# Kernel tuning notes

Hardware: AMD Instinct MI355X
Metric: run time of the kernel (lower is better)

Reference implementation:

```python
import jax, jax.numpy as jnp
import numpy as np

N = 100000
E = 1600000
IN_DIM = 512
HID = 64
OUT = 2


def gcn_conv(x, src, dst, W, b, n):
    # transform first (PyG GCNConv: x = x @ W, then propagate)
    xt = x @ W  # [n, d_out]
    # add self-loops
    loop = jnp.arange(n, dtype=src.dtype)
    src_sl = jnp.concatenate([src, loop])
    dst_sl = jnp.concatenate([dst, loop])
    # symmetric normalization: deg over destination (col) incl. self-loops
    ones = jnp.ones(src_sl.shape[0], dtype=xt.dtype)
    deg = jax.ops.segment_sum(ones, dst_sl, num_segments=n)
    dis = jnp.where(deg > 0, jax.lax.rsqrt(deg), 0.0)  # deg^-1/2, inf -> 0
    norm = dis[src_sl] * dis[dst_sl]  # [E+n]
    msgs = xt[src_sl] * norm[:, None]  # gather + scale
    out = jax.ops.segment_sum(msgs, dst_sl, num_segments=n)  # scatter-add
    return out + b


def setup_inputs() -> dict:
    key = jax.random.key(0)
    k0, k1, k2, k3, k4, k5 = jax.random.split(key, 6)
    x = jax.random.normal(k0, (N, IN_DIM), dtype=jnp.float32)
    edge_index = jax.random.randint(k1, (2, E), 0, N, dtype=jnp.int64)
    s1 = 1.0 / np.sqrt(IN_DIM)
    s2 = 1.0 / np.sqrt(HID)
    W1 = jax.random.uniform(k2, (IN_DIM, HID), jnp.float32, -s1, s1)
    b1 = jax.random.uniform(k3, (HID,), jnp.float32, -s1, s1)
    W2 = jax.random.uniform(k4, (HID, OUT), jnp.float32, -s2, s2)
    b2 = jax.random.uniform(k5, (OUT,), jnp.float32, -s2, s2)
    return {"x": x, "edge_index": edge_index, "W1": W1, "b1": b1, "W2": W2, "b2": b2}


def reference(x, edge_index, W1, b1, W2, b2):
    src, dst = edge_index[0], edge_index[1]
    h = gcn_conv(x, src, dst, W1, b1, N)
    h = jax.nn.relu(h)
    # dropout is identity in eval mode (training=False)
    h = gcn_conv(h, src, dst, W2, b2, N)
    return jax.nn.log_softmax(h, axis=1)
```

## Files before the change

### kernel.cpp

```cpp
#include <hip/hip_runtime.h>
#include <hip/hip_bf16.h>

#define NN 100000
#define EE 1600000
#define IN_DIM 512
#define HID 64
#define NB1 391
#define NCH 196
#define CHUNK 8192
#define NGEMM 1563

typedef __attribute__((ext_vector_type(8))) short bf16x8;
typedef __attribute__((ext_vector_type(4))) float f32x4;

static __device__ __forceinline__ short f2bf(float f) {
    __hip_bfloat16 h = __float2bfloat16(f);
    return *reinterpret_cast<short*>(&h);
}
static __device__ __forceinline__ float bf2f(unsigned short u) {
    union { unsigned int i; float f; } c; c.i = ((unsigned int)u) << 16;
    return c.f;
}

__global__ __launch_bounds__(256) void pack_hist_kernel(const float* __restrict__ W1,
                                                        bf16x8* __restrict__ W1p,
                                                        const int* __restrict__ dst,
                                                        int* __restrict__ cnt2d) {
    if (blockIdx.x < 16) {
        int t = blockIdx.x * 256 + threadIdx.x;
        int kstep = t >> 8;
        int kb = (t >> 6) & 3;
        int col = t & 63;
        int kbase = kstep * 32 + kb * 8;
        bf16x8 v;
#pragma unroll
        for (int j = 0; j < 8; ++j) v[j] = f2bf(W1[(size_t)(kbase + j) * HID + col]);
        W1p[t] = v;
    } else {
        __shared__ int h[NB1];
        const int c = blockIdx.x - 16;
        const int t = threadIdx.x;
        for (int i = t; i < NB1; i += 256) h[i] = 0;
        __syncthreads();
        const int base = c * CHUNK;
        for (int i = t; i < CHUNK; i += 256) {
            int e = base + i;
            if (e < EE) atomicAdd(&h[dst[e] >> 8], 1);
        }
        __syncthreads();
        for (int i = t; i < NB1; i += 256) cnt2d[c * NB1 + i] = h[i];
    }
}

__global__ __launch_bounds__(256) void scan1b_kernel(const int* __restrict__ cnt2d,
                                                     int* __restrict__ base2d,
                                                     int* __restrict__ coarse) {
    __shared__ int tot[NB1];
    __shared__ int off[NB1 + 1];
    const int t = threadIdx.x;
    for (int i = t; i < NB1; i += 256) {
        int s = 0;
        for (int c = 0; c < NCH; ++c) s += cnt2d[c * NB1 + i];
        tot[i] = s;
    }
    __syncthreads();
    if (t == 0) {
        int run = 0;
        for (int b = 0; b < NB1; ++b) { off[b] = run; run += tot[b]; }
        off[NB1] = run;
    }
    __syncthreads();
    for (int i = t; i < NB1; i += 256) {
        int run = off[i];
        for (int c = 0; c < NCH; ++c) {
            base2d[c * NB1 + i] = run;
            run += cnt2d[c * NB1 + i];
        }
    }
    for (int i = t; i <= NB1; i += 256) coarse[i] = off[i];
}

__global__ __launch_bounds__(256) void scatter1c_kernel(const int* __restrict__ src,
                                                        const int* __restrict__ dst,
                                                        const int* __restrict__ base2d,
                                                        unsigned int* __restrict__ pairs) {
    __shared__ int cur[NB1];
    const int t = threadIdx.x;
    for (int i = t; i < NB1; i += 256) cur[i] = base2d[blockIdx.x * NB1 + i];
    __syncthreads();
    const int base = blockIdx.x * CHUNK;
    for (int i = t; i < CHUNK; i += 256) {
        int e = base + i;
        if (e < EE) {
            int s = src[e], d = dst[e];
            int pos = atomicAdd(&cur[d >> 8], 1);
            pairs[pos] = ((unsigned int)s << 8) | (unsigned int)(d & 255);
        }
    }
}

__global__ __launch_bounds__(256) void sort_gemm_kernel(
        const unsigned int* __restrict__ pairs, const int* __restrict__ coarse,
        int* __restrict__ offsets, int* __restrict__ cursor,
        int* __restrict__ sorted_src, float* __restrict__ dis,
        const float* __restrict__ x, const bf16x8* __restrict__ W1p,
        unsigned short* __restrict__ xt1b) {
    if (blockIdx.x < NB1) {
        __shared__ int sdeg[256];
        __shared__ int sinc[256];
        __shared__ int scur[256];
        const int b = blockIdx.x;
        const int t = threadIdx.x;
        const int n0 = b << 8;
        const int nn = min(256, NN - n0);
        const int e0 = coarse[b], e1 = coarse[b + 1];

        sdeg[t] = 0;
        __syncthreads();
        for (int e = e0 + t; e < e1; e += 256)
            atomicAdd(&sdeg[pairs[e] & 255u], 1);
        __syncthreads();
        sinc[t] = sdeg[t];
        __syncthreads();
        for (int off = 1; off < 256; off <<= 1) {
            int v = (t >= off) ? sinc[t - off] : 0;
            __syncthreads();
            sinc[t] += v;
            __syncthreads();
        }
        int excl = sinc[t] - sdeg[t];
        scur[t] = excl;
        if (t < nn) {
            offsets[n0 + t] = e0 + excl;
            cursor[n0 + t]  = e0 + excl + sdeg[t];
            dis[n0 + t]     = rsqrtf((float)sdeg[t] + 1.0f);
        }
        __syncthreads();
        for (int e = e0 + t; e < e1; e += 256) {
            unsigned int p = pairs[e];
            int pos = atomicAdd(&scur[p & 255u], 1);
            sorted_src[e0 + pos] = (int)(p >> 8);
        }
    } else {
        const int gb = blockIdx.x - NB1;
        const int wave = threadIdx.x >> 6;
        const int lane = threadIdx.x & 63;
        const int r = lane & 15;
        const int kg = lane >> 4;
        const int row0 = gb * 64 + wave * 16;
        const int rowc = min(row0 + r, NN - 1);
        const float* xr = x + (size_t)rowc * IN_DIM;

        f32x4 acc[4] = {};
#pragma unroll
        for (int ks = 0; ks < 16; ++ks) {
            const int k0 = ks * 32 + kg * 8;
            float4 xa = *(const float4*)(xr + k0);
            float4 xb = *(const float4*)(xr + k0 + 4);
            bf16x8 a;
            a[0] = f2bf(xa.x); a[1] = f2bf(xa.y); a[2] = f2bf(xa.z); a[3] = f2bf(xa.w);
            a[4] = f2bf(xb.x); a[5] = f2bf(xb.y); a[6] = f2bf(xb.z); a[7] = f2bf(xb.w);
            const int bbase = (ks * 4 + kg) * 64;
#pragma unroll
            for (int cb = 0; cb < 4; ++cb) {
                bf16x8 bfr = W1p[bbase + cb * 16 + r];
                acc[cb] = __builtin_amdgcn_mfma_f32_16x16x32_bf16(a, bfr, acc[cb], 0, 0, 0);
            }
        }
#pragma unroll
        for (int cb = 0; cb < 4; ++cb) {
#pragma unroll
            for (int reg = 0; reg < 4; ++reg) {
                int ro = row0 + kg * 4 + reg;
                if (ro < NN) xt1b[(size_t)ro * HID + cb * 16 + r] =
                    (unsigned short)f2bf(acc[cb][reg]);
            }
        }
    }
}

__global__ __launch_bounds__(256) void agg1_fused_kernel(
        const int* __restrict__ offsets, const int* __restrict__ cursor,
        const int* __restrict__ sorted_src, const float* __restrict__ dis,
        const unsigned short* __restrict__ xt1b, const float* __restrict__ b1,
        const float* __restrict__ W2, float* __restrict__ xt2) {
    int node = blockIdx.x * 4 + (threadIdx.x >> 6);
    if (node >= NN) return;
    const int lane = threadIdx.x & 63;
    const int grp = lane >> 4;
    const int fl = lane & 15;
    const int beg = offsets[node], end = cursor[node];
    const float dd = dis[node];
    float acc0 = 0.f, acc1 = 0.f, acc2 = 0.f, acc3 = 0.f;

    for (int base = beg; base < end; base += 64) {
        int m = min(64, end - base);
        int s = 0;
        float nd = 0.f;
        if (lane < m) {
            s = sorted_src[base + lane];
            nd = dis[s];
        }
#pragma unroll 4
        for (int jj = 0; jj < m; jj += 4) {
            int j = jj + grp;
            int sj = __shfl(s, j);
            float nj = __shfl(nd, j);
            float w = (j < m) ? nj : 0.f;
            ushort4 v = *(const ushort4*)(xt1b + (size_t)sj * HID + fl * 4);
            acc0 += bf2f(v.x) * w;
            acc1 += bf2f(v.y) * w;
            acc2 += bf2f(v.z) * w;
            acc3 += bf2f(v.w) * w;
        }
    }
    acc0 += __shfl_xor(acc0, 16); acc0 += __shfl_xor(acc0, 32);
    acc1 += __shfl_xor(acc1, 16); acc1 += __shfl_xor(acc1, 32);
    acc2 += __shfl_xor(acc2, 16); acc2 += __shfl_xor(acc2, 32);
    acc3 += __shfl_xor(acc3, 16); acc3 += __shfl_xor(acc3, 32);

    ushort4 xs = *(const ushort4*)(xt1b + (size_t)node * HID + fl * 4);
    float4 bb = *(const float4*)(b1 + fl * 4);
    float d2 = dd * dd;
    float h0 = fmaxf(acc0 * dd + bf2f(xs.x) * d2 + bb.x, 0.f);
    float h1 = fmaxf(acc1 * dd + bf2f(xs.y) * d2 + bb.y, 0.f);
    float h2 = fmaxf(acc2 * dd + bf2f(xs.z) * d2 + bb.z, 0.f);
    float h3 = fmaxf(acc3 * dd + bf2f(xs.w) * d2 + bb.w, 0.f);

    float4 w01 = *(const float4*)(W2 + fl * 8);
    float4 w23 = *(const float4*)(W2 + fl * 8 + 4);
    float a0 = h0 * w01.x + h1 * w01.z + h2 * w23.x + h3 * w23.z;
    float a1 = h0 * w01.y + h1 * w01.w + h2 * w23.y + h3 * w23.w;
    a0 += __shfl_xor(a0, 1); a0 += __shfl_xor(a0, 2);
    a0 += __shfl_xor(a0, 4); a0 += __shfl_xor(a0, 8);
    a1 += __shfl_xor(a1, 1); a1 += __shfl_xor(a1, 2);
    a1 += __shfl_xor(a1, 4); a1 += __shfl_xor(a1, 8);
    if (lane == 0) *(float2*)(xt2 + (size_t)node * 2) = make_float2(a0, a1);
}

__global__ void agg2_final_kernel(const int* __restrict__ offsets, const int* __restrict__ cursor,
                                  const int* __restrict__ sorted_src,
                                  const float* __restrict__ dis,
                                  const float* __restrict__ xt2,
                                  const float* __restrict__ b2,
                                  float* __restrict__ out) {
    int node = blockIdx.x * 256 + threadIdx.x;
    if (node >= NN) return;
    int beg = offsets[node], end = cursor[node];
    float dd = dis[node];
    float d2 = dd * dd;
    float a0 = xt2[(size_t)node * 2 + 0] * d2;
    float a1 = xt2[(size_t)node * 2 + 1] * d2;
    for (int p = beg; p < end; ++p) {
        int s = sorted_src[p];
        float nrm = dis[s] * dd;
        float2 v = *(const float2*)(xt2 + (size_t)s * 2);
        a0 += v.x * nrm;
        a1 += v.y * nrm;
    }
    float v0 = a0 + b2[0], v1 = a1 + b2[1];
    float m = fmaxf(v0, v1);
    float lse = m + logf(expf(v0 - m) + expf(v1 - m));
    out[(size_t)node * 2 + 0] = v0 - lse;
    out[(size_t)node * 2 + 1] = v1 - lse;
}

extern "C" void kernel_launch(void* const* d_in, const int* in_sizes, int n_in,
                              void* d_out, int out_size, void* d_ws, size_t ws_size,
                              hipStream_t stream) {
    const float* x  = (const float*)d_in[0];
    const int* ei   = (const int*)d_in[1];
    const float* W1 = (const float*)d_in[2];
    const float* b1 = (const float*)d_in[3];
    const float* W2 = (const float*)d_in[4];
    const float* b2 = (const float*)d_in[5];
    const int* src = ei;
    const int* dst = ei + EE;
    float* out = (float*)d_out;

    unsigned short* xt1b = (unsigned short*)d_ws;
    float* dis        = (float*)(xt1b + (size_t)NN * HID);
    int*   offsets    = (int*)(dis + NN);
    int*   cursor     = offsets + NN;
    int*   sorted_src = cursor + NN;
    float* xt2        = (float*)(sorted_src + EE);
    bf16x8* W1p       = (bf16x8*)(xt2 + (size_t)NN * 2);
    int*   cnt2d      = (int*)(W1p + 4096);
    int*   base2d     = cnt2d + NCH * NB1;
    int*   coarse     = base2d + NCH * NB1;
    unsigned int* pairs = (unsigned int*)(coarse + NB1 + 1);

    pack_hist_kernel<<<16 + NCH, 256, 0, stream>>>(W1, W1p, dst, cnt2d);
    scan1b_kernel<<<1, 256, 0, stream>>>(cnt2d, base2d, coarse);
    scatter1c_kernel<<<NCH, 256, 0, stream>>>(src, dst, base2d, pairs);
    sort_gemm_kernel<<<NB1 + NGEMM, 256, 0, stream>>>(pairs, coarse, offsets, cursor,
                                                      sorted_src, dis, x, W1p, xt1b);
    agg1_fused_kernel<<<(NN + 3) / 4, 256, 0, stream>>>(offsets, cursor, sorted_src,
                                                        dis, xt1b, b1, W2, xt2);
    agg2_final_kernel<<<(NN + 255) / 256, 256, 0, stream>>>(offsets, cursor, sorted_src,
                                                            dis, xt2, b2, out);
}
```

Before: 182.7 us.

## Merge all stages into one cooperative persistent kernel with grid syncs

Replaces six kernel launches with a single cooperative kernel that separates stages with grid.sync. The GEMM tiles are split across the histogram, scatter and sort phases so the dense transform overlaps the edge-sorting work. The global prefix scan is dropped in favour of fixed per-bucket arenas of 5120 slots, with counts clamped to the arena size. This removes launch gaps and the serial single-block scan, at the cost of grid-sync overhead and a correctness risk if any bucket has more than 5120 edges.

```diff
diff --git a/kernel.cpp b/kernel.cpp
--- a/kernel.cpp
+++ b/kernel.cpp
@@ -1,5 +1,8 @@
 #include <hip/hip_runtime.h>
 #include <hip/hip_bf16.h>
+#include <hip/hip_cooperative_groups.h>
+
+namespace cg = cooperative_groups;
 
 #define NN 100000
 #define EE 1600000
@@ -9,6 +12,10 @@
 #define NCH 196
 #define CHUNK 8192
 #define NGEMM 1563
+#define ARENA 5120
+#define P1G 828
+#define P3G 400
+#define P4G (NGEMM - P1G - P3G)
 
 typedef __attribute__((ext_vector_type(8))) short bf16x8;
 typedef __attribute__((ext_vector_type(4))) float f32x4;
@@ -22,73 +29,82 @@
     return c.f;
 }
 
-__global__ __launch_bounds__(256) void pack_hist_kernel(const float* __restrict__ W1,
-                                                        bf16x8* __restrict__ W1p,
-                                                        const int* __restrict__ dst,
-                                                        int* __restrict__ cnt2d) {
-    if (blockIdx.x < 16) {
-        int t = blockIdx.x * 256 + threadIdx.x;
-        int kstep = t >> 8;
-        int kb = (t >> 6) & 3;
-        int col = t & 63;
-        int kbase = kstep * 32 + kb * 8;
-        bf16x8 v;
-#pragma unroll
-        for (int j = 0; j < 8; ++j) v[j] = f2bf(W1[(size_t)(kbase + j) * HID + col]);
-        W1p[t] = v;
-    } else {
-        __shared__ int h[NB1];
-        const int c = blockIdx.x - 16;
-        const int t = threadIdx.x;
-        for (int i = t; i < NB1; i += 256) h[i] = 0;
-        __syncthreads();
-        const int base = c * CHUNK;
-        for (int i = t; i < CHUNK; i += 256) {
-            int e = base + i;
-            if (e < EE) atomicAdd(&h[dst[e] >> 8], 1);
-        }
-        __syncthreads();
-        for (int i = t; i < NB1; i += 256) cnt2d[c * NB1 + i] = h[i];
-    }
-}
-
-__global__ __launch_bounds__(256) void scan1b_kernel(const int* __restrict__ cnt2d,
-                                                     int* __restrict__ base2d,
-                                                     int* __restrict__ coarse) {
-    __shared__ int tot[NB1];
-    __shared__ int off[NB1 + 1];
+
+__device__ __forceinline__ void do_pack(int t, const float* __restrict__ W1,
+                                        bf16x8* __restrict__ W1p) {
+    int kstep = t >> 8;
+    int kb = (t >> 6) & 3;
+    int col = t & 63;
+    int kbase = kstep * 32 + kb * 8;
+    bf16x8 v;
+#pragma unroll
+    for (int j = 0; j < 8; ++j) v[j] = f2bf(W1[(size_t)(kbase + j) * HID + col]);
+    W1p[t] = v;
+}
+
+__device__ __forceinline__ void do_gemm(int gb, const float* __restrict__ x,
+                                        const bf16x8* __restrict__ W1p,
+                                        unsigned short* __restrict__ xt1b) {
+    const int wave = threadIdx.x >> 6;
+    const int lane = threadIdx.x & 63;
+    const int r = lane & 15;
+    const int kg = lane >> 4;
+    const int row0 = gb * 64 + wave * 16;
+    const int rowc = min(row0 + r, NN - 1);
+    const float* xr = x + (size_t)rowc * IN_DIM;
+
+    f32x4 acc[4] = {};
+#pragma unroll
+    for (int ks = 0; ks < 16; ++ks) {
+        const int k0 = ks * 32 + kg * 8;
+        float4 xa = *(const float4*)(xr + k0);
+        float4 xb = *(const float4*)(xr + k0 + 4);
+        bf16x8 a;
+        a[0] = f2bf(xa.x); a[1] = f2bf(xa.y); a[2] = f2bf(xa.z); a[3] = f2bf(xa.w);
+        a[4] = f2bf(xb.x); a[5] = f2bf(xb.y); a[6] = f2bf(xb.z); a[7] = f2bf(xb.w);
+        const int bbase = (ks * 4 + kg) * 64;
+#pragma unroll
+        for (int cb = 0; cb < 4; ++cb) {
+            bf16x8 bfr = W1p[bbase + cb * 16 + r];
+            acc[cb] = __builtin_amdgcn_mfma_f32_16x16x32_bf16(a, bfr, acc[cb], 0, 0, 0);
+        }
+    }
+#pragma unroll
+    for (int cb = 0; cb < 4; ++cb) {
+#pragma unroll
+        for (int reg = 0; reg < 4; ++reg) {
+            int ro = row0 + kg * 4 + reg;
+            if (ro < NN) xt1b[(size_t)ro * HID + cb * 16 + r] =
+                (unsigned short)f2bf(acc[cb][reg]);
+        }
+    }
+}
+
+__device__ __forceinline__ void do_hist(int c, const int* __restrict__ dst,
+                                        int* __restrict__ cnt2d, int* shm) {
+    int* h = shm;
     const int t = threadIdx.x;
-    for (int i = t; i < NB1; i += 256) {
-        int s = 0;
-        for (int c = 0; c < NCH; ++c) s += cnt2d[c * NB1 + i];
-        tot[i] = s;
-    }
-    __syncthreads();
-    if (t == 0) {
-        int run = 0;
-        for (int b = 0; b < NB1; ++b) { off[b] = run; run += tot[b]; }
-        off[NB1] = run;
-    }
-    __syncthreads();
-    for (int i = t; i < NB1; i += 256) {
-        int run = off[i];
-        for (int c = 0; c < NCH; ++c) {
-            base2d[c * NB1 + i] = run;
-            run += cnt2d[c * NB1 + i];
-        }
-    }
-    for (int i = t; i <= NB1; i += 256) coarse[i] = off[i];
-}
-
-__global__ __launch_bounds__(256) void scatter1c_kernel(const int* __restrict__ src,
-                                                        const int* __restrict__ dst,
-                                                        const int* __restrict__ base2d,
-                                                        unsigned int* __restrict__ pairs) {
-    __shared__ int cur[NB1];
+    for (int i = t; i < NB1; i += 256) h[i] = 0;
+    __syncthreads();
+    const int base = c * CHUNK;
+    for (int i = t; i < CHUNK; i += 256) {
+        int e = base + i;
+        if (e < EE) atomicAdd(&h[dst[e] >> 8], 1);
+    }
+    __syncthreads();
+    for (int i = t; i < NB1; i += 256) cnt2d[c * NB1 + i] = h[i];
+    __syncthreads();
+}
+
+__device__ __forceinline__ void do_scatter(int c, const int* __restrict__ src,
+                                           const int* __restrict__ dst,
+                                           const int* __restrict__ base2d,
+                                           unsigned int* __restrict__ pairs, int* shm) {
+    int* cur = shm;
     const int t = threadIdx.x;
-    for (int i = t; i < NB1; i += 256) cur[i] = base2d[blockIdx.x * NB1 + i];
-    __syncthreads();
-    const int base = blockIdx.x * CHUNK;
+    for (int i = t; i < NB1; i += 256) cur[i] = i * ARENA + base2d[c * NB1 + i];
+    __syncthreads();
+    const int base = c * CHUNK;
     for (int i = t; i < CHUNK; i += 256) {
         int e = base + i;
         if (e < EE) {
@@ -97,94 +113,58 @@
             pairs[pos] = ((unsigned int)s << 8) | (unsigned int)(d & 255);
         }
     }
-}
-
-__global__ __launch_bounds__(256) void sort_gemm_kernel(
-        const unsigned int* __restrict__ pairs, const int* __restrict__ coarse,
-        int* __restrict__ offsets, int* __restrict__ cursor,
-        int* __restrict__ sorted_src, float* __restrict__ dis,
-        const float* __restrict__ x, const bf16x8* __restrict__ W1p,
-        unsigned short* __restrict__ xt1b) {
-    if (blockIdx.x < NB1) {
-        __shared__ int sdeg[256];
-        __shared__ int sinc[256];
-        __shared__ int scur[256];
-        const int b = blockIdx.x;
-        const int t = threadIdx.x;
-        const int n0 = b << 8;
-        const int nn = min(256, NN - n0);
-        const int e0 = coarse[b], e1 = coarse[b + 1];
-
-        sdeg[t] = 0;
+    __syncthreads();
+}
+
+__device__ __forceinline__ void do_sort(int b, const unsigned int* __restrict__ pairs,
+                                        const int* __restrict__ edge_cnt,
+                                        int* __restrict__ offsets, int* __restrict__ cursor,
+                                        int* __restrict__ sorted_src,
+                                        float* __restrict__ dis, int* shm) {
+    int* sdeg = shm;
+    int* sinc = shm + 256;
+    int* scur = shm + 512;
+    const int t = threadIdx.x;
+    const int n0 = b << 8;
+    const int nn = min(256, NN - n0);
+    const int e0 = b * ARENA;
+    const int e1 = e0 + min(edge_cnt[b], ARENA);
+
+    sdeg[t] = 0;
+    __syncthreads();
+    for (int e = e0 + t; e < e1; e += 256)
+        atomicAdd(&sdeg[pairs[e] & 255u], 1);
+    __syncthreads();
+    sinc[t] = sdeg[t];
+    __syncthreads();
+    for (int off = 1; off < 256; off <<= 1) {
+        int v = (t >= off) ? sinc[t - off] : 0;
         __syncthreads();
-        for (int e = e0 + t; e < e1; e += 256)
-            atomicAdd(&sdeg[pairs[e] & 255u], 1);
+        sinc[t] += v;
         __syncthreads();
-        sinc[t] = sdeg[t];
-        __syncthreads();
-        for (int off = 1; off < 256; off <<= 1) {
-            int v = (t >= off) ? sinc[t - off] : 0;
-            __syncthreads();
-            sinc[t] += v;
-            __syncthreads();
-        }
-        int excl = sinc[t] - sdeg[t];
-        scur[t] = excl;
-        if (t < nn) {
-            offsets[n0 + t] = e0 + excl;
-            cursor[n0 + t]  = e0 + excl + sdeg[t];
-            dis[n0 + t]     = rsqrtf((float)sdeg[t] + 1.0f);
-        }
-        __syncthreads();
-        for (int e = e0 + t; e < e1; e += 256) {
-            unsigned int p = pairs[e];
-            int pos = atomicAdd(&scur[p & 255u], 1);
-            sorted_src[e0 + pos] = (int)(p >> 8);
-        }
-    } else {
-        const int gb = blockIdx.x - NB1;
-        const int wave = threadIdx.x >> 6;
-        const int lane = threadIdx.x & 63;
-        const int r = lane & 15;
-        const int kg = lane >> 4;
-        const int row0 = gb * 64 + wave * 16;
-        const int rowc = min(row0 + r, NN - 1);
-        const float* xr = x + (size_t)rowc * IN_DIM;
-
-        f32x4 acc[4] = {};
-#pragma unroll
-        for (int ks = 0; ks < 16; ++ks) {
-            const int k0 = ks * 32 + kg * 8;
-            float4 xa = *(const float4*)(xr + k0);
-            float4 xb = *(const float4*)(xr + k0 + 4);
-            bf16x8 a;
-            a[0] = f2bf(xa.x); a[1] = f2bf(xa.y); a[2] = f2bf(xa.z); a[3] = f2bf(xa.w);
-            a[4] = f2bf(xb.x); a[5] = f2bf(xb.y); a[6] = f2bf(xb.z); a[7] = f2bf(xb.w);
-            const int bbase = (ks * 4 + kg) * 64;
-#pragma unroll
-            for (int cb = 0; cb < 4; ++cb) {
-                bf16x8 bfr = W1p[bbase + cb * 16 + r];
-                acc[cb] = __builtin_amdgcn_mfma_f32_16x16x32_bf16(a, bfr, acc[cb], 0, 0, 0);
-            }
-        }
-#pragma unroll
-        for (int cb = 0; cb < 4; ++cb) {
-#pragma unroll
-            for (int reg = 0; reg < 4; ++reg) {
-                int ro = row0 + kg * 4 + reg;
-                if (ro < NN) xt1b[(size_t)ro * HID + cb * 16 + r] =
-                    (unsigned short)f2bf(acc[cb][reg]);
-            }
-        }
-    }
-}
-
-__global__ __launch_bounds__(256) void agg1_fused_kernel(
-        const int* __restrict__ offsets, const int* __restrict__ cursor,
-        const int* __restrict__ sorted_src, const float* __restrict__ dis,
-        const unsigned short* __restrict__ xt1b, const float* __restrict__ b1,
-        const float* __restrict__ W2, float* __restrict__ xt2) {
-    int node = blockIdx.x * 4 + (threadIdx.x >> 6);
+    }
+    int excl = sinc[t] - sdeg[t];
+    scur[t] = excl;
+    if (t < nn) {
+        offsets[n0 + t] = e0 + excl;
+        cursor[n0 + t]  = e0 + excl + sdeg[t];
+        dis[n0 + t]     = rsqrtf((float)sdeg[t] + 1.0f);
+    }
+    __syncthreads();
+    for (int e = e0 + t; e < e1; e += 256) {
+        unsigned int p = pairs[e];
+        int pos = atomicAdd(&scur[p & 255u], 1);
+        sorted_src[e0 + pos] = (int)(p >> 8);
+    }
+    __syncthreads();
+}
+
+__device__ __forceinline__ void do_agg1(int q, const int* __restrict__ offsets,
+        const int* __restrict__ cursor, const int* __restrict__ sorted_src,
+        const float* __restrict__ dis, const unsigned short* __restrict__ xt1b,
+        const float* __restrict__ b1, const float* __restrict__ W2,
+        float* __restrict__ xt2) {
+    int node = q * 4 + (threadIdx.x >> 6);
     if (node >= NN) return;
     const int lane = threadIdx.x & 63;
     const int grp = lane >> 4;
@@ -238,14 +218,10 @@
     if (lane == 0) *(float2*)(xt2 + (size_t)node * 2) = make_float2(a0, a1);
 }
 
-__global__ void agg2_final_kernel(const int* __restrict__ offsets, const int* __restrict__ cursor,
-                                  const int* __restrict__ sorted_src,
-                                  const float* __restrict__ dis,
-                                  const float* __restrict__ xt2,
-                                  const float* __restrict__ b2,
-                                  float* __restrict__ out) {
-    int node = blockIdx.x * 256 + threadIdx.x;
-    if (node >= NN) return;
+__device__ __forceinline__ void do_agg2(int node, const int* __restrict__ offsets,
+        const int* __restrict__ cursor, const int* __restrict__ sorted_src,
+        const float* __restrict__ dis, const float* __restrict__ xt2,
+        const float* __restrict__ b2, float* __restrict__ out) {
     int beg = offsets[node], end = cursor[node];
     float dd = dis[node];
     float d2 = dd * dd;
@@ -263,6 +239,62 @@
     float lse = m + logf(expf(v0 - m) + expf(v1 - m));
     out[(size_t)node * 2 + 0] = v0 - lse;
     out[(size_t)node * 2 + 1] = v1 - lse;
+}
+
+__global__ __launch_bounds__(256, 4) void gcn_coop(
+        const float* __restrict__ x, const int* __restrict__ src,
+        const int* __restrict__ dst, const float* __restrict__ W1,
+        const float* __restrict__ b1, const float* __restrict__ W2,
+        const float* __restrict__ b2, float* __restrict__ out,
+        unsigned short* __restrict__ xt1b, float* __restrict__ dis,
+        int* __restrict__ offsets, int* __restrict__ cursor,
+        float* __restrict__ xt2, bf16x8* __restrict__ W1p,
+        int* __restrict__ cnt2d, int* __restrict__ base2d,
+        int* __restrict__ edge_cnt, int* __restrict__ sorted_src,
+        unsigned int* __restrict__ pairs) {
+    cg::grid_group grid = cg::this_grid();
+    __shared__ int shm[768];
+    const int nb = gridDim.x;
+    const int nthreads = nb * 256;
+    const int gt = blockIdx.x * 256 + threadIdx.x;
+
+    for (int t = gt; t < 4096; t += nthreads) do_pack(t, W1, W1p);
+    grid.sync();
+
+    for (int u = blockIdx.x; u < NCH + P1G; u += nb) {
+        if (u < NCH) do_hist(u, dst, cnt2d, shm);
+        else         do_gemm(u - NCH, x, W1p, xt1b);
+    }
+    grid.sync();
+
+    for (int i = gt; i < NB1; i += nthreads) {
+        int run = 0;
+        for (int c = 0; c < NCH; ++c) {
+            base2d[c * NB1 + i] = run;
+            run += cnt2d[c * NB1 + i];
+        }
+        edge_cnt[i] = run;
+    }
+    grid.sync();
+
+    for (int u = blockIdx.x; u < NCH + P3G; u += nb) {
+        if (u < NCH) do_scatter(u, src, dst, base2d, pairs, shm);
+        else         do_gemm(P1G + (u - NCH), x, W1p, xt1b);
+    }
+    grid.sync();
+
+    for (int u = blockIdx.x; u < NB1 + P4G; u += nb) {
+        if (u < NB1) do_sort(u, pairs, edge_cnt, offsets, cursor, sorted_src, dis, shm);
+        else         do_gemm(P1G + P3G + (u - NB1), x, W1p, xt1b);
+    }
+    grid.sync();
+
+    for (int q = blockIdx.x; q < (NN + 3) / 4; q += nb)
+        do_agg1(q, offsets, cursor, sorted_src, dis, xt1b, b1, W2, xt2);
+    grid.sync();
+
+    for (int n = gt; n < NN; n += nthreads)
+        do_agg2(n, offsets, cursor, sorted_src, dis, xt2, b2, out);
 }
 
 extern "C" void kernel_launch(void* const* d_in, const int* in_sizes, int n_in,
@@ -282,21 +314,26 @@
     float* dis        = (float*)(xt1b + (size_t)NN * HID);
     int*   offsets    = (int*)(dis + NN);
     int*   cursor     = offsets + NN;
-    int*   sorted_src = cursor + NN;
-    float* xt2        = (float*)(sorted_src + EE);
+    float* xt2        = (float*)(cursor + NN);
     bf16x8* W1p       = (bf16x8*)(xt2 + (size_t)NN * 2);
     int*   cnt2d      = (int*)(W1p + 4096);
     int*   base2d     = cnt2d + NCH * NB1;
-    int*   coarse     = base2d + NCH * NB1;
-    unsigned int* pairs = (unsigned int*)(coarse + NB1 + 1);
-
-    pack_hist_kernel<<<16 + NCH, 256, 0, stream>>>(W1, W1p, dst, cnt2d);
-    scan1b_kernel<<<1, 256, 0, stream>>>(cnt2d, base2d, coarse);
-    scatter1c_kernel<<<NCH, 256, 0, stream>>>(src, dst, base2d, pairs);
-    sort_gemm_kernel<<<NB1 + NGEMM, 256, 0, stream>>>(pairs, coarse, offsets, cursor,
-                                                      sorted_src, dis, x, W1p, xt1b);
-    agg1_fused_kernel<<<(NN + 3) / 4, 256, 0, stream>>>(offsets, cursor, sorted_src,
-                                                        dis, xt1b, b1, W2, xt2);
-    agg2_final_kernel<<<(NN + 255) / 256, 256, 0, stream>>>(offsets, cursor, sorted_src,
-                                                            dis, xt2, b2, out);
-}
+    int*   edge_cnt   = base2d + NCH * NB1;
+    int*   sorted_src = edge_cnt + NB1;
+    unsigned int* pairs = (unsigned int*)(sorted_src + (size_t)NB1 * ARENA);
+
+    int nbpc = 0;
+    if (hipOccupancyMaxActiveBlocksPerMultiprocessor(&nbpc, gcn_coop, 256, 0) != hipSuccess
+        || nbpc < 1) nbpc = 2;
+    if (nbpc > 8) nbpc = 8;
+    int grid = 256 * nbpc;
+    if (grid > 2048) grid = 2048;
+
+    void* args[] = {
+        (void*)&x, (void*)&src, (void*)&dst, (void*)&W1, (void*)&b1, (void*)&W2,
+        (void*)&b2, (void*)&out, (void*)&xt1b, (void*)&dis, (void*)&offsets,
+        (void*)&cursor, (void*)&xt2, (void*)&W1p, (void*)&cnt2d, (void*)&base2d,
+        (void*)&edge_cnt, (void*)&sorted_src, (void*)&pairs
+    };
+    hipLaunchCooperativeKernel((void*)gcn_coop, dim3(grid), dim3(256), args, 0, stream);
+}
```

New measurement: 680.7 us (median of 2 runs). 3.73x slower.

## Drop serial scan kernel via fixed-size bucket arenas and split GEMM across scatter/sort

Applied to the files above, without the earlier changes.

Removes the single-block prefix-scan kernel: each scatter block now computes its own per-bucket offset by scanning the histogram column. Buckets are placed in fixed-capacity arenas of ARENA slots instead of packed offsets. Part of the bf16 MFMA feature GEMM is moved into the scatter launch so it runs alongside scatter, and the rest stays with the sort. This removes a serial launch and balances GEMM work across two kernels. The risk is that edges beyond arena capacity are silently dropped, which is only safe for near-uniform destination distributions.

```diff
diff --git a/kernel.cpp b/kernel.cpp
--- a/kernel.cpp
+++ b/kernel.cpp
@@ -9,6 +9,9 @@
 #define NCH 196
 #define CHUNK 8192
 #define NGEMM 1563
+#define ARENA 5120
+#define GA 800
+#define GB (NGEMM - GA)
 
 typedef __attribute__((ext_vector_type(8))) short bf16x8;
 typedef __attribute__((ext_vector_type(4))) float f32x4;
@@ -20,6 +23,44 @@
 static __device__ __forceinline__ float bf2f(unsigned short u) {
     union { unsigned int i; float f; } c; c.i = ((unsigned int)u) << 16;
     return c.f;
+}
+
+__device__ __forceinline__ void do_gemm(int gb, const float* __restrict__ x,
+                                        const bf16x8* __restrict__ W1p,
+                                        unsigned short* __restrict__ xt1b) {
+    const int wave = threadIdx.x >> 6;
+    const int lane = threadIdx.x & 63;
+    const int r = lane & 15;
+    const int kg = lane >> 4;
+    const int row0 = gb * 64 + wave * 16;
+    const int rowc = min(row0 + r, NN - 1);
+    const float* xr = x + (size_t)rowc * IN_DIM;
+
+    f32x4 acc[4] = {};
+#pragma unroll
+    for (int ks = 0; ks < 16; ++ks) {
+        const int k0 = ks * 32 + kg * 8;
+        float4 xa = *(const float4*)(xr + k0);
+        float4 xb = *(const float4*)(xr + k0 + 4);
+        bf16x8 a;
+        a[0] = f2bf(xa.x); a[1] = f2bf(xa.y); a[2] = f2bf(xa.z); a[3] = f2bf(xa.w);
+        a[4] = f2bf(xb.x); a[5] = f2bf(xb.y); a[6] = f2bf(xb.z); a[7] = f2bf(xb.w);
+        const int bbase = (ks * 4 + kg) * 64;
+#pragma unroll
+        for (int cb = 0; cb < 4; ++cb) {
+            bf16x8 bfr = W1p[bbase + cb * 16 + r];
+            acc[cb] = __builtin_amdgcn_mfma_f32_16x16x32_bf16(a, bfr, acc[cb], 0, 0, 0);
+        }
+    }
+#pragma unroll
+    for (int cb = 0; cb < 4; ++cb) {
+#pragma unroll
+        for (int reg = 0; reg < 4; ++reg) {
+            int ro = row0 + kg * 4 + reg;
+            if (ro < NN) xt1b[(size_t)ro * HID + cb * 16 + r] =
+                (unsigned short)f2bf(acc[cb][reg]);
+        }
+    }
 }
 
 __global__ __launch_bounds__(256) void pack_hist_kernel(const float* __restrict__ W1,
@@ -52,55 +93,45 @@
     }
 }
 
-__global__ __launch_bounds__(256) void scan1b_kernel(const int* __restrict__ cnt2d,
-                                                     int* __restrict__ base2d,
-                                                     int* __restrict__ coarse) {
-    __shared__ int tot[NB1];
-    __shared__ int off[NB1 + 1];
-    const int t = threadIdx.x;
-    for (int i = t; i < NB1; i += 256) {
-        int s = 0;
-        for (int c = 0; c < NCH; ++c) s += cnt2d[c * NB1 + i];
-        tot[i] = s;
-    }
-    __syncthreads();
-    if (t == 0) {
-        int run = 0;
-        for (int b = 0; b < NB1; ++b) { off[b] = run; run += tot[b]; }
-        off[NB1] = run;
-    }
-    __syncthreads();
-    for (int i = t; i < NB1; i += 256) {
-        int run = off[i];
-        for (int c = 0; c < NCH; ++c) {
-            base2d[c * NB1 + i] = run;
-            run += cnt2d[c * NB1 + i];
-        }
-    }
-    for (int i = t; i <= NB1; i += 256) coarse[i] = off[i];
-}
-
-__global__ __launch_bounds__(256) void scatter1c_kernel(const int* __restrict__ src,
-                                                        const int* __restrict__ dst,
-                                                        const int* __restrict__ base2d,
-                                                        unsigned int* __restrict__ pairs) {
-    __shared__ int cur[NB1];
-    const int t = threadIdx.x;
-    for (int i = t; i < NB1; i += 256) cur[i] = base2d[blockIdx.x * NB1 + i];
-    __syncthreads();
-    const int base = blockIdx.x * CHUNK;
-    for (int i = t; i < CHUNK; i += 256) {
-        int e = base + i;
-        if (e < EE) {
-            int s = src[e], d = dst[e];
-            int pos = atomicAdd(&cur[d >> 8], 1);
-            pairs[pos] = ((unsigned int)s << 8) | (unsigned int)(d & 255);
-        }
+__global__ __launch_bounds__(256) void scatter_gemm_kernel(
+        const int* __restrict__ src, const int* __restrict__ dst,
+        const int* __restrict__ cnt2d, unsigned int* __restrict__ pairs,
+        int* __restrict__ edge_cnt,
+        const float* __restrict__ x, const bf16x8* __restrict__ W1p,
+        unsigned short* __restrict__ xt1b) {
+    if (blockIdx.x < NCH) {
+        __shared__ int cur[NB1];
+        const int c = blockIdx.x;
+        const int t = threadIdx.x;
+        for (int i = t; i < NB1; i += 256) {
+            int run = 0, pp = 0;
+            for (int c2 = 0; c2 < NCH; ++c2) {
+                int v = cnt2d[c2 * NB1 + i];
+                if (c2 == c) pp = run;
+                run += v;
+            }
+            cur[i] = i * ARENA + pp;
+            if (c == 0) edge_cnt[i] = run;
+        }
+        __syncthreads();
+        const int base = c * CHUNK;
+        for (int i = t; i < CHUNK; i += 256) {
+            int e = base + i;
+            if (e < EE) {
+                int s = src[e], d = dst[e];
+                int bkt = d >> 8;
+                int pos = atomicAdd(&cur[bkt], 1);
+                if (pos < (bkt + 1) * ARENA)
+                    pairs[pos] = ((unsigned int)s << 8) | (unsigned int)(d & 255);
+            }
+        }
+    } else {
+        do_gemm(blockIdx.x - NCH, x, W1p, xt1b);
     }
 }
 
 __global__ __launch_bounds__(256) void sort_gemm_kernel(
-        const unsigned int* __restrict__ pairs, const int* __restrict__ coarse,
+        const unsigned int* __restrict__ pairs, const int* __restrict__ edge_cnt,
         int* __restrict__ offsets, int* __restrict__ cursor,
         int* __restrict__ sorted_src, float* __restrict__ dis,
         const float* __restrict__ x, const bf16x8* __restrict__ W1p,
@@ -113,7 +144,8 @@
         const int t = threadIdx.x;
         const int n0 = b << 8;
         const int nn = min(256, NN - n0);
-        const int e0 = coarse[b], e1 = coarse[b + 1];
+        const int e0 = b * ARENA;
+        const int e1 = e0 + min(edge_cnt[b], ARENA);
 
         sdeg[t] = 0;
         __syncthreads();
@@ -142,40 +174,7 @@
             sorted_src[e0 + pos] = (int)(p >> 8);
         }
     } else {
-        const int gb = blockIdx.x - NB1;
-        const int wave = threadIdx.x >> 6;
-        const int lane = threadIdx.x & 63;
-        const int r = lane & 15;
-        const int kg = lane >> 4;
-        const int row0 = gb * 64 + wave * 16;
-        const int rowc = min(row0 + r, NN - 1);
-        const float* xr = x + (size_t)rowc * IN_DIM;
-
-        f32x4 acc[4] = {};
-#pragma unroll
-        for (int ks = 0; ks < 16; ++ks) {
-            const int k0 = ks * 32 + kg * 8;
-            float4 xa = *(const float4*)(xr + k0);
-            float4 xb = *(const float4*)(xr + k0 + 4);
-            bf16x8 a;
-            a[0] = f2bf(xa.x); a[1] = f2bf(xa.y); a[2] = f2bf(xa.z); a[3] = f2bf(xa.w);
-            a[4] = f2bf(xb.x); a[5] = f2bf(xb.y); a[6] = f2bf(xb.z); a[7] = f2bf(xb.w);
-            const int bbase = (ks * 4 + kg) * 64;
-#pragma unroll
-            for (int cb = 0; cb < 4; ++cb) {
-                bf16x8 bfr = W1p[bbase + cb * 16 + r];
-                acc[cb] = __builtin_amdgcn_mfma_f32_16x16x32_bf16(a, bfr, acc[cb], 0, 0, 0);
-            }
-        }
-#pragma unroll
-        for (int cb = 0; cb < 4; ++cb) {
-#pragma unroll
-            for (int reg = 0; reg < 4; ++reg) {
-                int ro = row0 + kg * 4 + reg;
-                if (ro < NN) xt1b[(size_t)ro * HID + cb * 16 + r] =
-                    (unsigned short)f2bf(acc[cb][reg]);
-            }
-        }
+        do_gemm(GA + (blockIdx.x - NB1), x, W1p, xt1b);
     }
 }
 
@@ -282,19 +281,18 @@
     float* dis        = (float*)(xt1b + (size_t)NN * HID);
     int*   offsets    = (int*)(dis + NN);
     int*   cursor     = offsets + NN;
-    int*   sorted_src = cursor + NN;
-    float* xt2        = (float*)(sorted_src + EE);
+    float* xt2        = (float*)(cursor + NN);
     bf16x8* W1p       = (bf16x8*)(xt2 + (size_t)NN * 2);
     int*   cnt2d      = (int*)(W1p + 4096);
-    int*   base2d     = cnt2d + NCH * NB1;
-    int*   coarse     = base2d + NCH * NB1;
-    unsigned int* pairs = (unsigned int*)(coarse + NB1 + 1);
+    int*   edge_cnt   = cnt2d + NCH * NB1;
+    int*   sorted_src = edge_cnt + NB1;
+    unsigned int* pairs = (unsigned int*)(sorted_src + (size_t)NB1 * ARENA);
 
     pack_hist_kernel<<<16 + NCH, 256, 0, stream>>>(W1, W1p, dst, cnt2d);
-    scan1b_kernel<<<1, 256, 0, stream>>>(cnt2d, base2d, coarse);
-    scatter1c_kernel<<<NCH, 256, 0, stream>>>(src, dst, base2d, pairs);
-    sort_gemm_kernel<<<NB1 + NGEMM, 256, 0, stream>>>(pairs, coarse, offsets, cursor,
-                                                      sorted_src, dis, x, W1p, xt1b);
+    scatter_gemm_kernel<<<NCH + GA, 256, 0, stream>>>(src, dst, cnt2d, pairs, edge_cnt,
+                                                      x, W1p, xt1b);
+    sort_gemm_kernel<<<NB1 + GB, 256, 0, stream>>>(pairs, edge_cnt, offsets, cursor,
+                                                   sorted_src, dis, x, W1p, xt1b);
     agg1_fused_kernel<<<(NN + 3) / 4, 256, 0, stream>>>(offsets, cursor, sorted_src,
                                                         dis, xt1b, b1, W2, xt2);
     agg2_final_kernel<<<(NN + 255) / 256, 256, 0, stream>>>(offsets, cursor, sorted_src,
```

Result: faster. 165.0 us (-9.7%).
